# Optimization experiments

Hardware: AMD Instinct MI355X
Metric: run time of the kernel (lower is better)

## Reference

```python
import jax, jax.numpy as jnp
import numpy as np

N, E = 50000, 1600000
D_IN, H, N_REL, D_OUT = 518, 256, 10, 128


def setup_inputs() -> dict:
    key = jax.random.key(0)
    ks = jax.random.split(key, 20)
    def lin(k, fan_in, fan_out):
        bound = 1.0 / np.sqrt(fan_in)
        kw, kb = jax.random.split(k)
        W = jax.random.uniform(kw, (fan_in, fan_out), jnp.float32, -bound, bound)
        b = jax.random.uniform(kb, (fan_out,), jnp.float32, -bound, bound)
        return W, b
    x = jax.random.normal(ks[0], (N, D_IN), jnp.float32)
    edge_index = jax.random.randint(ks[1], (2, E), 0, N, jnp.int32)
    edge_attr = jax.random.randint(ks[2], (E,), 0, N_REL, jnp.int32)
    W_enc1, b_enc1 = lin(ks[3], D_IN, H)
    W_enc2, b_enc2 = lin(ks[4], H, H)
    emb_table = jax.random.normal(ks[5], (N_REL, H // 4), jnp.float32)
    W_g1, b_g1 = lin(ks[6], H, H)
    W_g2, b_g2 = lin(ks[7], H, H)
    W_g3, b_g3 = lin(ks[8], H, H)
    W_h1, b_h1 = lin(ks[9], H, H // 2)
    W_h2, b_h2 = lin(ks[10], H // 2, D_OUT)
    return dict(x=x, edge_index=edge_index, edge_attr=edge_attr,
                W_enc1=W_enc1, b_enc1=b_enc1, W_enc2=W_enc2, b_enc2=b_enc2,
                emb_table=emb_table,
                W_g1=W_g1, b_g1=b_g1, W_g2=W_g2, b_g2=b_g2, W_g3=W_g3, b_g3=b_g3,
                W_h1=W_h1, b_h1=b_h1, W_h2=W_h2, b_h2=b_h2)


def reference(x, edge_index, edge_attr,
              W_enc1, b_enc1, W_enc2, b_enc2, emb_table,
              W_g1, b_g1, W_g2, b_g2, W_g3, b_g3,
              W_h1, b_h1, W_h2, b_h2):
    src, dst = edge_index[0], edge_index[1]
    n = x.shape[0]
    # GCN symmetric normalization with self-loops: deg = 1 + in-degree
    deg = 1.0 + jax.ops.segment_sum(jnp.ones_like(src, jnp.float32), dst, num_segments=n)
    dis = deg ** -0.5                       # [N]
    norm_e = dis[src] * dis[dst]            # [E] edge norm
    self_norm = (dis * dis)[:, None]        # [N,1] self-loop norm

    def gcn(h, W, b):
        hw = h @ W                           # [N,H]
        agg = jax.ops.segment_sum(hw[src] * norm_e[:, None], dst, num_segments=n)
        return agg + hw * self_norm + b

    # node encoder (dropout is identity in eval)
    h = jax.nn.relu(x @ W_enc1 + b_enc1) @ W_enc2 + b_enc2
    _edge_emb = emb_table[edge_attr]         # computed as in original (unused downstream)
    h = jax.nn.relu(gcn(h, W_g1, b_g1))
    h = jax.nn.relu(gcn(h, W_g2, b_g2))
    h = jax.nn.relu(gcn(h, W_g3, b_g3))
    graph_repr = jnp.mean(h, axis=0, keepdims=True)   # batch=None path -> [1,H]
    out = jax.nn.relu(graph_repr @ W_h1 + b_h1) @ W_h2 + b_h2
    return out
```

## Files before the change

### kernel.cpp

```cpp
#include <hip/hip_runtime.h>

#define D_IN 518
#define HD 256
#define KP1 544

typedef __attribute__((ext_vector_type(8))) short bf16x8;
typedef __attribute__((ext_vector_type(4))) float f32x4;
typedef __attribute__((ext_vector_type(4), aligned(4))) float float4u;
typedef __attribute__((ext_vector_type(8))) unsigned short ushort8v;

__device__ __forceinline__ float bf2f(unsigned short u) {
  union { unsigned int i; float f; } v; v.i = ((unsigned int)u) << 16; return v.f;
}
__device__ __forceinline__ unsigned short f2bf(float f) {
  union { float f; unsigned int i; } v; v.f = f;
  unsigned int r = (v.i + 0x7FFFu + ((v.i >> 16) & 1u)) >> 16;
  return (unsigned short)r;
}
__device__ __forceinline__ float rl_f(float x, int j) {
  return __int_as_float(__builtin_amdgcn_readlane(__float_as_int(x), j));
}

__global__ void k_canary(float* __restrict__ out, float code) {
  out[threadIdx.x] = code;
}


__global__ void k_hist(const int* __restrict__ dst, int E, int* __restrict__ cnt) {
  int e = blockIdx.x * blockDim.x + threadIdx.x;
  if (e < E) atomicAdd(&cnt[dst[e]], 1);
}

__global__ void k_blocksum(const int* __restrict__ cnt, int n, int* __restrict__ bsum) {
  __shared__ int red[256];
  const int t = threadIdx.x;
  int v = blockIdx.x * 256 + t;
  red[t] = (v < n) ? cnt[v] : 0;
  __syncthreads();
  for (int d = 128; d > 0; d >>= 1) {
    if (t < d) red[t] += red[t + d];
    __syncthreads();
  }
  if (t == 0) bsum[blockIdx.x] = red[0];
}

__global__ void k_scan_mid(const int* __restrict__ bsum, int nb, int* __restrict__ bex) {
  __shared__ int s[256];
  const int t = threadIdx.x;
  int x = (t < nb) ? bsum[t] : 0;
  s[t] = x;
  __syncthreads();
  for (int d = 1; d < 256; d <<= 1) {
    int v = (t >= d) ? s[t - d] : 0;
    __syncthreads();
    s[t] += v;
    __syncthreads();
  }
  if (t < nb) bex[t] = s[t] - x;
}

__global__ void k_off(const int* __restrict__ cnt, int n, const int* __restrict__ bex,
                      int* __restrict__ off, int* __restrict__ cursor,
                      float* __restrict__ dis) {
  __shared__ int s[256];
  const int t = threadIdx.x;
  const int v = blockIdx.x * 256 + t;
  int c = (v < n) ? cnt[v] : 0;
  s[t] = c;
  __syncthreads();
  for (int d = 1; d < 256; d <<= 1) {
    int x = (t >= d) ? s[t - d] : 0;
    __syncthreads();
    s[t] += x;
    __syncthreads();
  }
  if (v < n) {
    int incl = bex[blockIdx.x] + s[t];
    off[v + 1] = incl;
    cursor[v] = incl - c;
    dis[v] = 1.0f / sqrtf(1.0f + (float)c);
    if (v == 0) off[0] = 0;
  }
}

__global__ void k_fill_range(const int* __restrict__ src, const int* __restrict__ dst, int E,
                             int* __restrict__ cursor, int* __restrict__ csr,
                             int lo, int hi) {
  int e = blockIdx.x * blockDim.x + threadIdx.x;
  if (e < E) {
    int d = dst[e];
    if (d >= lo && d < hi) {
      int p = atomicAdd(&cursor[d], 1);
      csr[p] = src[e];
    }
  }
}


__global__ void k_wt(const float* __restrict__ W, int K, int N, int Kp,
                     unsigned short* __restrict__ Wt) {
  int idx = blockIdx.x * blockDim.x + threadIdx.x;
  if (idx < N * Kp) {
    int n = idx / Kp, k = idx - n * Kp;
    Wt[idx] = (k < K) ? f2bf(W[k * N + n]) : (unsigned short)0;
  }
}

__global__ void k_wt4(const float* __restrict__ a, const float* __restrict__ b,
                      const float* __restrict__ c, const float* __restrict__ d,
                      unsigned short* __restrict__ oa, unsigned short* __restrict__ ob,
                      unsigned short* __restrict__ oc, unsigned short* __restrict__ od) {
  const float* W = (blockIdx.y == 0) ? a : (blockIdx.y == 1) ? b : (blockIdx.y == 2) ? c : d;
  unsigned short* O = (blockIdx.y == 0) ? oa : (blockIdx.y == 1) ? ob : (blockIdx.y == 2) ? oc : od;
  int idx = blockIdx.x * blockDim.x + threadIdx.x;
  int n = idx >> 8, k = idx & 255;
  O[idx] = f2bf(W[k * HD + n]);
}


__global__ __launch_bounds__(256, 2)
void k_gemm_bt(const unsigned short* __restrict__ A, int lda, int M, int K,
               const unsigned short* __restrict__ Bt, int ldb,
               const float* __restrict__ bias, int do_relu,
               unsigned short* __restrict__ C, int ldc) {
  __shared__ unsigned short As[128 * 40];
  __shared__ unsigned short Bs[128 * 40];
  const int tid = threadIdx.x;
  const int lane = tid & 63, wave = tid >> 6;
  const int q = lane >> 4, l15 = lane & 15;
  const int wm = (wave & 1) * 64, wn = (wave >> 1) * 64;
  const int m0 = blockIdx.x * 128, n0 = blockIdx.y * 128;

  f32x4 acc[4][4];
#pragma unroll
  for (int i = 0; i < 4; i++)
#pragma unroll
    for (int j = 0; j < 4; j++) acc[i][j] = f32x4{0.f, 0.f, 0.f, 0.f};

  const int r0 = tid >> 2, kb = tid & 3;
  int gmA0 = m0 + r0;       if (gmA0 >= M) gmA0 = M - 1;
  int gmA1 = m0 + r0 + 64;  if (gmA1 >= M) gmA1 = M - 1;
  const unsigned short* Arow0 = A + (size_t)gmA0 * lda;
  const unsigned short* Arow1 = A + (size_t)gmA1 * lda;
  const unsigned short* Brow0 = Bt + (size_t)(n0 + r0) * ldb;
  const unsigned short* Brow1 = Bt + (size_t)(n0 + r0 + 64) * ldb;
  unsigned short* lA0 = &As[r0 * 40 + kb * 8];
  unsigned short* lA1 = &As[(r0 + 64) * 40 + kb * 8];
  unsigned short* lB0 = &Bs[r0 * 40 + kb * 8];
  unsigned short* lB1 = &Bs[(r0 + 64) * 40 + kb * 8];

  for (int k0 = 0; k0 < K; k0 += 32) {
    __syncthreads();
    const int gk = k0 + kb * 8;
    *(bf16x8*)lA0 = *(const bf16x8*)(Arow0 + gk);
    *(bf16x8*)lA1 = *(const bf16x8*)(Arow1 + gk);
    *(bf16x8*)lB0 = *(const bf16x8*)(Brow0 + gk);
    *(bf16x8*)lB1 = *(const bf16x8*)(Brow1 + gk);
    __syncthreads();

    bf16x8 af[4], bfr[4];
#pragma unroll
    for (int i = 0; i < 4; i++)
      af[i] = *(const bf16x8*)(&As[(wm + i * 16 + l15) * 40 + q * 8]);
#pragma unroll
    for (int j = 0; j < 4; j++)
      bfr[j] = *(const bf16x8*)(&Bs[(wn + j * 16 + l15) * 40 + q * 8]);
#pragma unroll
    for (int i = 0; i < 4; i++)
#pragma unroll
      for (int j = 0; j < 4; j++)
        acc[i][j] = __builtin_amdgcn_mfma_f32_16x16x32_bf16(af[i], bfr[j], acc[i][j], 0, 0, 0);
  }

#pragma unroll
  for (int j = 0; j < 4; j++) {
    const int col = n0 + wn + j * 16 + l15;
    const float bv = bias ? bias[col] : 0.f;
#pragma unroll
    for (int i = 0; i < 4; i++) {
#pragma unroll
      for (int rg = 0; rg < 4; rg++) {
        int gr = m0 + wm + i * 16 + q * 4 + rg;
        if (gr < M) {
          float v = acc[i][j][rg] + bv;
          if (do_relu) v = fmaxf(v, 0.f);
          C[(size_t)gr * ldc + col] = f2bf(v);
        }
      }
    }
  }
}


__global__ __launch_bounds__(256, 2)
void k_gemm_f32in(const float* __restrict__ A, int lda, int M, int Kreal, int Kloop,
                  const unsigned short* __restrict__ Bt, int ldb,
                  const float* __restrict__ bias, int do_relu,
                  unsigned short* __restrict__ C, int ldc) {
  __shared__ unsigned short As[128 * 40];
  __shared__ unsigned short Bs[128 * 40];
  const int tid = threadIdx.x;
  const int lane = tid & 63, wave = tid >> 6;
  const int q = lane >> 4, l15 = lane & 15;
  const int wm = (wave & 1) * 64, wn = (wave >> 1) * 64;
  const int m0 = blockIdx.x * 128, n0 = blockIdx.y * 128;

  f32x4 acc[4][4];
#pragma unroll
  for (int i = 0; i < 4; i++)
#pragma unroll
    for (int j = 0; j < 4; j++) acc[i][j] = f32x4{0.f, 0.f, 0.f, 0.f};

  const int r0 = tid >> 2, kb = tid & 3;
  int gmA0 = m0 + r0;       if (gmA0 >= M) gmA0 = M - 1;
  int gmA1 = m0 + r0 + 64;  if (gmA1 >= M) gmA1 = M - 1;
  const float* Arow0 = A + (size_t)gmA0 * lda;
  const float* Arow1 = A + (size_t)gmA1 * lda;
  const unsigned short* Brow0 = Bt + (size_t)(n0 + r0) * ldb;
  const unsigned short* Brow1 = Bt + (size_t)(n0 + r0 + 64) * ldb;
  unsigned short* lA0 = &As[r0 * 40 + kb * 8];
  unsigned short* lA1 = &As[(r0 + 64) * 40 + kb * 8];
  unsigned short* lB0 = &Bs[r0 * 40 + kb * 8];
  unsigned short* lB1 = &Bs[(r0 + 64) * 40 + kb * 8];

  for (int k0 = 0; k0 < Kloop; k0 += 32) {
    __syncthreads();
    const int gk = k0 + kb * 8;
    if (gk + 8 <= Kreal) {
      float4u a0 = *(const float4u*)(Arow0 + gk);
      float4u a1 = *(const float4u*)(Arow0 + gk + 4);
      float4u b0 = *(const float4u*)(Arow1 + gk);
      float4u b1 = *(const float4u*)(Arow1 + gk + 4);
      bf16x8 t0, t1;
      t0[0] = (short)f2bf(a0.x); t0[1] = (short)f2bf(a0.y);
      t0[2] = (short)f2bf(a0.z); t0[3] = (short)f2bf(a0.w);
      t0[4] = (short)f2bf(a1.x); t0[5] = (short)f2bf(a1.y);
      t0[6] = (short)f2bf(a1.z); t0[7] = (short)f2bf(a1.w);
      t1[0] = (short)f2bf(b0.x); t1[1] = (short)f2bf(b0.y);
      t1[2] = (short)f2bf(b0.z); t1[3] = (short)f2bf(b0.w);
      t1[4] = (short)f2bf(b1.x); t1[5] = (short)f2bf(b1.y);
      t1[6] = (short)f2bf(b1.z); t1[7] = (short)f2bf(b1.w);
      *(bf16x8*)lA0 = t0;
      *(bf16x8*)lA1 = t1;
    } else {
      bf16x8 t0, t1;
#pragma unroll
      for (int t = 0; t < 8; t++) {
        int kk = gk + t;
        t0[t] = (short)((kk < Kreal) ? f2bf(Arow0[kk]) : (unsigned short)0);
        t1[t] = (short)((kk < Kreal) ? f2bf(Arow1[kk]) : (unsigned short)0);
      }
      *(bf16x8*)lA0 = t0;
      *(bf16x8*)lA1 = t1;
    }
    *(bf16x8*)lB0 = *(const bf16x8*)(Brow0 + gk);
    *(bf16x8*)lB1 = *(const bf16x8*)(Brow1 + gk);
    __syncthreads();

    bf16x8 af[4], bfr[4];
#pragma unroll
    for (int i = 0; i < 4; i++)
      af[i] = *(const bf16x8*)(&As[(wm + i * 16 + l15) * 40 + q * 8]);
#pragma unroll
    for (int j = 0; j < 4; j++)
      bfr[j] = *(const bf16x8*)(&Bs[(wn + j * 16 + l15) * 40 + q * 8]);
#pragma unroll
    for (int i = 0; i < 4; i++)
#pragma unroll
      for (int j = 0; j < 4; j++)
        acc[i][j] = __builtin_amdgcn_mfma_f32_16x16x32_bf16(af[i], bfr[j], acc[i][j], 0, 0, 0);
  }

#pragma unroll
  for (int j = 0; j < 4; j++) {
    const int col = n0 + wn + j * 16 + l15;
    const float bv = bias ? bias[col] : 0.f;
#pragma unroll
    for (int i = 0; i < 4; i++) {
#pragma unroll
      for (int rg = 0; rg < 4; rg++) {
        int gr = m0 + wm + i * 16 + q * 4 + rg;
        if (gr < M) {
          float v = acc[i][j][rg] + bv;
          if (do_relu) v = fmaxf(v, 0.f);
          C[(size_t)gr * ldc + col] = f2bf(v);
        }
      }
    }
  }
}


__global__ __launch_bounds__(256)
void k_agg(const unsigned short* __restrict__ hw,
           const int* __restrict__ off, const int* __restrict__ csr,
           const float* __restrict__ dis,
           const float* __restrict__ bias,
           unsigned short* __restrict__ hout, int n) {
  const int wave = threadIdx.x >> 6, lane = threadIdx.x & 63;
  const int v = blockIdx.x * 4 + wave;
  if (v >= n) return;
  const int half = lane >> 5, lc = lane & 31;
  const unsigned short* hwl = hw + lc * 8;
  float a[8];
#pragma unroll
  for (int k = 0; k < 8; ++k) a[k] = 0.f;

  const int e0 = off[v], e1 = off[v + 1];
  for (int e = e0; e < e1; e += 64) {
    int cnt = e1 - e; if (cnt > 64) cnt = 64;
    int sidx = 0; float w = 0.f;
    if (e + lane < e1) { sidx = csr[e + lane]; w = dis[sidx]; }
    int j = 0;
    for (; j + 8 <= cnt; j += 8) {
      int s[4]; float wv[4];
#pragma unroll
      for (int p = 0; p < 4; ++p) {
        int sl = __builtin_amdgcn_readlane(sidx, j + 2 * p);
        int sh = __builtin_amdgcn_readlane(sidx, j + 2 * p + 1);
        float wl = rl_f(w, j + 2 * p);
        float wh = rl_f(w, j + 2 * p + 1);
        s[p]  = half ? sh : sl;
        wv[p] = half ? wh : wl;
      }
      ushort8v h[4];
#pragma unroll
      for (int p = 0; p < 4; ++p)
        h[p] = *(const ushort8v*)(hwl + (size_t)s[p] * HD);
#pragma unroll
      for (int p = 0; p < 4; ++p)
#pragma unroll
        for (int k = 0; k < 8; ++k)
          a[k] += wv[p] * bf2f(h[p][k]);
    }
    for (; j < cnt; j += 2) {
      int sl = __builtin_amdgcn_readlane(sidx, j);
      float wl = rl_f(w, j);
      int sh; float wh;
      if (j + 1 < cnt) { sh = __builtin_amdgcn_readlane(sidx, j + 1); wh = rl_f(w, j + 1); }
      else             { sh = sl; wh = 0.f; }
      int s   = half ? sh : sl;
      float ww = half ? wh : wl;
      ushort8v hv = *(const ushort8v*)(hwl + (size_t)s * HD);
#pragma unroll
      for (int k = 0; k < 8; ++k) a[k] += ww * bf2f(hv[k]);
    }
  }

#pragma unroll
  for (int k = 0; k < 8; ++k) a[k] += __shfl_xor(a[k], 32, 64);

  if (half == 0) {
    const float dv = dis[v], sn = dv * dv;
    ushort8v hs = *(const ushort8v*)(hwl + (size_t)v * HD);
    const int c = lc * 8;
    ushort8v o;
#pragma unroll
    for (int k = 0; k < 8; ++k)
      o[k] = f2bf(fmaxf(dv * a[k] + sn * bf2f(hs[k]) + bias[c + k], 0.f));
    *(ushort8v*)(hout + (size_t)v * HD + c) = o;
  }
}


__global__ void k_colsum(const unsigned short* __restrict__ h, int n, float* __restrict__ gsum) {
  const int t = threadIdx.x;
  const int per = (n + gridDim.x - 1) / gridDim.x;
  const int rs = blockIdx.x * per;
  int re = rs + per; if (re > n) re = n;
  float s = 0.f;
  for (int r = rs; r < re; ++r) s += bf2f(h[(size_t)r * HD + t]);
  atomicAdd(&gsum[t], s);
}

__global__ void k_head(const float* __restrict__ gsum, float invN,
                       const float* __restrict__ Wh1, const float* __restrict__ bh1,
                       const float* __restrict__ Wh2, const float* __restrict__ bh2,
                       float* __restrict__ out) {
  __shared__ float g[256];
  __shared__ float t1[128];
  const int t = threadIdx.x;
  g[t] = gsum[t] * invN;
  g[t + 128] = gsum[t + 128] * invN;
  __syncthreads();
  float s = bh1[t];
  for (int k = 0; k < 256; ++k) s += g[k] * Wh1[k * 128 + t];
  t1[t] = fmaxf(s, 0.f);
  __syncthreads();
  float o = bh2[t];
  for (int j = 0; j < 128; ++j) o += t1[j] * Wh2[j * 128 + t];
  out[t] = o;
}


extern "C" void kernel_launch(void* const* d_in, const int* in_sizes, int n_in,
                              void* d_out, int out_size, void* d_ws, size_t ws_size,
                              hipStream_t stream) {
  float* outp = (float*)d_out;

  const float* x   = (const float*)d_in[0];
  const int* ei    = (const int*)d_in[1];
  const float* W1  = (const float*)d_in[3];
  const float* b1  = (const float*)d_in[4];
  const float* W2  = (const float*)d_in[5];
  const float* b2  = (const float*)d_in[6];
  const float* Wg1 = (const float*)d_in[8];
  const float* bg1 = (const float*)d_in[9];
  const float* Wg2 = (const float*)d_in[10];
  const float* bg2 = (const float*)d_in[11];
  const float* Wg3 = (const float*)d_in[12];
  const float* bg3 = (const float*)d_in[13];
  const float* Wh1 = (const float*)d_in[14];
  const float* bh1 = (const float*)d_in[15];
  const float* Wh2 = (const float*)d_in[16];
  const float* bh2 = (const float*)d_in[17];

  const int n = 50000;
  const int E = 1600000;
  const int nb = (n + 255) / 256;
  const int* srcp = ei;
  const int* dstp = ei + E;

  char* p = (char*)d_ws;
  size_t used = 0;
  auto alloc = [&](size_t bytes) -> char* {
    char* r = p; size_t rb = (bytes + 255) & ~((size_t)255);
    p += rb; used += rb; return r;
  };
  int*   cnt    = (int*)alloc((size_t)n * 4);
  int*   off    = (int*)alloc((size_t)(n + 1) * 4);
  int*   cursor = (int*)alloc((size_t)n * 4);
  float* dis    = (float*)alloc((size_t)n * 4);
  int*   bsum   = (int*)alloc((size_t)nb * 4);
  int*   bex    = (int*)alloc((size_t)nb * 4);
  float* gsum   = (float*)alloc(256 * 4);
  int*   csr    = (int*)alloc((size_t)E * 4);
  unsigned short* W1t  = (unsigned short*)alloc((size_t)HD * KP1 * 2);
  unsigned short* W2t  = (unsigned short*)alloc((size_t)HD * HD * 2);
  unsigned short* Wg1t = (unsigned short*)alloc((size_t)HD * HD * 2);
  unsigned short* Wg2t = (unsigned short*)alloc((size_t)HD * HD * 2);
  unsigned short* Wg3t = (unsigned short*)alloc((size_t)HD * HD * 2);
  unsigned short* P    = (unsigned short*)alloc((size_t)n * HD * 2);
  unsigned short* Q    = (unsigned short*)alloc((size_t)n * HD * 2);

  if (used > ws_size) { k_canary<<<1, 128, 0, stream>>>(outp, 90000.0f); return; }

  hipMemsetAsync(cnt, 0, (size_t)n * 4, stream);
  hipMemsetAsync(gsum, 0, 256 * 4, stream);

  k_hist<<<(E + 255) / 256, 256, 0, stream>>>(dstp, E, cnt);
  k_blocksum<<<nb, 256, 0, stream>>>(cnt, n, bsum);
  k_scan_mid<<<1, 256, 0, stream>>>(bsum, nb, bex);
  k_off<<<nb, 256, 0, stream>>>(cnt, n, bex, off, cursor, dis);
  {
    const int NPASS = 4, span = (n + NPASS - 1) / NPASS;
    for (int i = 0; i < NPASS; ++i) {
      int lo = i * span, hi = lo + span; if (hi > n) hi = n;
      k_fill_range<<<(E + 255) / 256, 256, 0, stream>>>(srcp, dstp, E, cursor, csr, lo, hi);
    }
  }

  k_wt<<<(HD * KP1 + 255) / 256, 256, 0, stream>>>(W1, D_IN, HD, KP1, W1t);
  {
    dim3 g4(HD * HD / 256, 4);
    k_wt4<<<g4, 256, 0, stream>>>(W2, Wg1, Wg2, Wg3, W2t, Wg1t, Wg2t, Wg3t);
  }

  dim3 gg((n + 127) / 128, HD / 128);
  const int ab = (n + 3) / 4;

  k_gemm_f32in<<<gg, 256, 0, stream>>>(x, D_IN, n, D_IN, KP1, W1t, KP1, b1, 1, P, HD);
  k_gemm_bt<<<gg, 256, 0, stream>>>(P, HD, n, HD, W2t, HD, b2, 0, Q, HD);
  k_gemm_bt<<<gg, 256, 0, stream>>>(Q, HD, n, HD, Wg1t, HD, nullptr, 0, P, HD);
  k_agg<<<ab, 256, 0, stream>>>(P, off, csr, dis, bg1, Q, n);
  k_gemm_bt<<<gg, 256, 0, stream>>>(Q, HD, n, HD, Wg2t, HD, nullptr, 0, P, HD);
  k_agg<<<ab, 256, 0, stream>>>(P, off, csr, dis, bg2, Q, n);
  k_gemm_bt<<<gg, 256, 0, stream>>>(Q, HD, n, HD, Wg3t, HD, nullptr, 0, P, HD);
  k_agg<<<ab, 256, 0, stream>>>(P, off, csr, dis, bg3, Q, n);

  k_colsum<<<256, 256, 0, stream>>>(Q, n, gsum);
  k_head<<<1, 128, 0, stream>>>(gsum, 1.0f / (float)n, Wh1, bh1, Wh2, bh2, outp);
}
```

Before: 893.1 us.

## Fold source-degree scaling into GEMM epilogue and simplify aggregation with 16-bit CSR

```diff
diff --git a/kernel.cpp b/kernel.cpp
--- a/kernel.cpp
+++ b/kernel.cpp
@@ -7,7 +7,8 @@
 typedef __attribute__((ext_vector_type(8))) short bf16x8;
 typedef __attribute__((ext_vector_type(4))) float f32x4;
 typedef __attribute__((ext_vector_type(4), aligned(4))) float float4u;
-typedef __attribute__((ext_vector_type(8))) unsigned short ushort8v;
+typedef __attribute__((ext_vector_type(2))) unsigned int uint2v;
+typedef __attribute__((ext_vector_type(4))) unsigned short ushort4v;
 
 __device__ __forceinline__ float bf2f(unsigned short u) {
   union { unsigned int i; float f; } v; v.i = ((unsigned int)u) << 16; return v.f;
@@ -17,9 +18,6 @@
   unsigned int r = (v.i + 0x7FFFu + ((v.i >> 16) & 1u)) >> 16;
   return (unsigned short)r;
 }
-__device__ __forceinline__ float rl_f(float x, int j) {
-  return __int_as_float(__builtin_amdgcn_readlane(__float_as_int(x), j));
-}
 
 __global__ void k_canary(float* __restrict__ out, float code) {
   out[threadIdx.x] = code;
@@ -27,8 +25,14 @@
 
 
 __global__ void k_hist(const int* __restrict__ dst, int E, int* __restrict__ cnt) {
-  int e = blockIdx.x * blockDim.x + threadIdx.x;
-  if (e < E) atomicAdd(&cnt[dst[e]], 1);
+  int e = (blockIdx.x * blockDim.x + threadIdx.x) * 4;
+  if (e < E) {
+    int4 d = *(const int4*)(dst + e);
+    atomicAdd(&cnt[d.x], 1);
+    atomicAdd(&cnt[d.y], 1);
+    atomicAdd(&cnt[d.z], 1);
+    atomicAdd(&cnt[d.w], 1);
+  }
 }
 
 __global__ void k_blocksum(const int* __restrict__ cnt, int n, int* __restrict__ bsum) {
@@ -84,15 +88,16 @@
 }
 
 __global__ void k_fill_range(const int* __restrict__ src, const int* __restrict__ dst, int E,
-                             int* __restrict__ cursor, int* __restrict__ csr,
+                             int* __restrict__ cursor, unsigned short* __restrict__ csr,
                              int lo, int hi) {
-  int e = blockIdx.x * blockDim.x + threadIdx.x;
+  int e = (blockIdx.x * blockDim.x + threadIdx.x) * 4;
   if (e < E) {
-    int d = dst[e];
-    if (d >= lo && d < hi) {
-      int p = atomicAdd(&cursor[d], 1);
-      csr[p] = src[e];
-    }
+    int4 d = *(const int4*)(dst + e);
+    int4 s = *(const int4*)(src + e);
+    if (d.x >= lo && d.x < hi) csr[atomicAdd(&cursor[d.x], 1)] = (unsigned short)s.x;
+    if (d.y >= lo && d.y < hi) csr[atomicAdd(&cursor[d.y], 1)] = (unsigned short)s.y;
+    if (d.z >= lo && d.z < hi) csr[atomicAdd(&cursor[d.z], 1)] = (unsigned short)s.z;
+    if (d.w >= lo && d.w < hi) csr[atomicAdd(&cursor[d.w], 1)] = (unsigned short)s.w;
   }
 }
 
@@ -121,7 +126,8 @@
 __global__ __launch_bounds__(256, 2)
 void k_gemm_bt(const unsigned short* __restrict__ A, int lda, int M, int K,
                const unsigned short* __restrict__ Bt, int ldb,
-               const float* __restrict__ bias, int do_relu,
+               const float* __restrict__ bias, const float* __restrict__ rowscale,
+               int do_relu,
                unsigned short* __restrict__ C, int ldc) {
   __shared__ unsigned short As[128 * 40];
   __shared__ unsigned short Bs[128 * 40];
@@ -182,7 +188,9 @@
       for (int rg = 0; rg < 4; rg++) {
         int gr = m0 + wm + i * 16 + q * 4 + rg;
         if (gr < M) {
-          float v = acc[i][j][rg] + bv;
+          float v = acc[i][j][rg];
+          if (rowscale) v *= rowscale[gr];
+          v += bv;
           if (do_relu) v = fmaxf(v, 0.f);
           C[(size_t)gr * ldc + col] = f2bf(v);
         }
@@ -293,73 +301,76 @@
 
 __global__ __launch_bounds__(256)
 void k_agg(const unsigned short* __restrict__ hw,
-           const int* __restrict__ off, const int* __restrict__ csr,
+           const int* __restrict__ off, const unsigned short* __restrict__ csr,
            const float* __restrict__ dis,
            const float* __restrict__ bias,
            unsigned short* __restrict__ hout, int n) {
   const int wave = threadIdx.x >> 6, lane = threadIdx.x & 63;
   const int v = blockIdx.x * 4 + wave;
   if (v >= n) return;
-  const int half = lane >> 5, lc = lane & 31;
-  const unsigned short* hwl = hw + lc * 8;
-  float a[8];
-#pragma unroll
-  for (int k = 0; k < 8; ++k) a[k] = 0.f;
+  const int cb = lane << 2;
+  float a0 = 0.f, a1 = 0.f, a2 = 0.f, a3 = 0.f;
 
   const int e0 = off[v], e1 = off[v + 1];
   for (int e = e0; e < e1; e += 64) {
     int cnt = e1 - e; if (cnt > 64) cnt = 64;
-    int sidx = 0; float w = 0.f;
-    if (e + lane < e1) { sidx = csr[e + lane]; w = dis[sidx]; }
+    int sidx = 0;
+    if (lane < cnt) sidx = (int)csr[e + lane];
     int j = 0;
     for (; j + 8 <= cnt; j += 8) {
-      int s[4]; float wv[4];
-#pragma unroll
-      for (int p = 0; p < 4; ++p) {
-        int sl = __builtin_amdgcn_readlane(sidx, j + 2 * p);
-        int sh = __builtin_amdgcn_readlane(sidx, j + 2 * p + 1);
-        float wl = rl_f(w, j + 2 * p);
-        float wh = rl_f(w, j + 2 * p + 1);
-        s[p]  = half ? sh : sl;
-        wv[p] = half ? wh : wl;
-      }
-      ushort8v h[4];
-#pragma unroll
-      for (int p = 0; p < 4; ++p)
-        h[p] = *(const ushort8v*)(hwl + (size_t)s[p] * HD);
-#pragma unroll
-      for (int p = 0; p < 4; ++p)
-#pragma unroll
-        for (int k = 0; k < 8; ++k)
-          a[k] += wv[p] * bf2f(h[p][k]);
-    }
-    for (; j < cnt; j += 2) {
-      int sl = __builtin_amdgcn_readlane(sidx, j);
-      float wl = rl_f(w, j);
-      int sh; float wh;
-      if (j + 1 < cnt) { sh = __builtin_amdgcn_readlane(sidx, j + 1); wh = rl_f(w, j + 1); }
-      else             { sh = sl; wh = 0.f; }
-      int s   = half ? sh : sl;
-      float ww = half ? wh : wl;
-      ushort8v hv = *(const ushort8v*)(hwl + (size_t)s * HD);
-#pragma unroll
-      for (int k = 0; k < 8; ++k) a[k] += ww * bf2f(hv[k]);
-    }
-  }
-
-#pragma unroll
-  for (int k = 0; k < 8; ++k) a[k] += __shfl_xor(a[k], 32, 64);
-
-  if (half == 0) {
-    const float dv = dis[v], sn = dv * dv;
-    ushort8v hs = *(const ushort8v*)(hwl + (size_t)v * HD);
-    const int c = lc * 8;
-    ushort8v o;
-#pragma unroll
-    for (int k = 0; k < 8; ++k)
-      o[k] = f2bf(fmaxf(dv * a[k] + sn * bf2f(hs[k]) + bias[c + k], 0.f));
-    *(ushort8v*)(hout + (size_t)v * HD + c) = o;
-  }
+      uint2v d[8];
+#pragma unroll
+      for (int p = 0; p < 8; ++p) {
+        int sp = __builtin_amdgcn_readlane(sidx, j + p);
+        const unsigned short* rowb = hw + ((size_t)sp << 8);
+        d[p] = *(const uint2v*)(rowb + cb);
+      }
+#pragma unroll
+      for (int p = 0; p < 8; ++p) {
+        a0 += __uint_as_float(d[p][0] << 16);
+        a1 += __uint_as_float(d[p][0] & 0xFFFF0000u);
+        a2 += __uint_as_float(d[p][1] << 16);
+        a3 += __uint_as_float(d[p][1] & 0xFFFF0000u);
+      }
+    }
+    if (j < cnt) {
+      uint2v d[8];
+#pragma unroll
+      for (int p = 0; p < 8; ++p) {
+        if (j + p < cnt) {
+          int sp = __builtin_amdgcn_readlane(sidx, j + p);
+          const unsigned short* rowb = hw + ((size_t)sp << 8);
+          d[p] = *(const uint2v*)(rowb + cb);
+        }
+      }
+#pragma unroll
+      for (int p = 0; p < 8; ++p) {
+        if (j + p < cnt) {
+          a0 += __uint_as_float(d[p][0] << 16);
+          a1 += __uint_as_float(d[p][0] & 0xFFFF0000u);
+          a2 += __uint_as_float(d[p][1] << 16);
+          a3 += __uint_as_float(d[p][1] & 0xFFFF0000u);
+        }
+      }
+    }
+  }
+
+  {
+    const unsigned short* rowb = hw + ((size_t)v << 8);
+    uint2v ds_ = *(const uint2v*)(rowb + cb);
+    a0 += __uint_as_float(ds_[0] << 16);
+    a1 += __uint_as_float(ds_[0] & 0xFFFF0000u);
+    a2 += __uint_as_float(ds_[1] << 16);
+    a3 += __uint_as_float(ds_[1] & 0xFFFF0000u);
+  }
+  const float dv = dis[v];
+  const float4u bv = *(const float4u*)(bias + cb);
+  ushort4v o;
+  o[0] = f2bf(fmaxf(dv * a0 + bv.x, 0.f));
+  o[1] = f2bf(fmaxf(dv * a1 + bv.y, 0.f));
+  o[2] = f2bf(fmaxf(dv * a2 + bv.z, 0.f));
+  o[3] = f2bf(fmaxf(dv * a3 + bv.w, 0.f));
+  *(ushort4v*)(hout + ((size_t)v << 8) + cb) = o;
 }
 
 
@@ -434,7 +445,7 @@
   int*   bsum   = (int*)alloc((size_t)nb * 4);
   int*   bex    = (int*)alloc((size_t)nb * 4);
   float* gsum   = (float*)alloc(256 * 4);
-  int*   csr    = (int*)alloc((size_t)E * 4);
+  unsigned short* csr = (unsigned short*)alloc((size_t)E * 2);
   unsigned short* W1t  = (unsigned short*)alloc((size_t)HD * KP1 * 2);
   unsigned short* W2t  = (unsigned short*)alloc((size_t)HD * HD * 2);
   unsigned short* Wg1t = (unsigned short*)alloc((size_t)HD * HD * 2);
@@ -448,15 +459,15 @@
   hipMemsetAsync(cnt, 0, (size_t)n * 4, stream);
   hipMemsetAsync(gsum, 0, 256 * 4, stream);
 
-  k_hist<<<(E + 255) / 256, 256, 0, stream>>>(dstp, E, cnt);
+  k_hist<<<(E / 4 + 255) / 256, 256, 0, stream>>>(dstp, E, cnt);
   k_blocksum<<<nb, 256, 0, stream>>>(cnt, n, bsum);
   k_scan_mid<<<1, 256, 0, stream>>>(bsum, nb, bex);
   k_off<<<nb, 256, 0, stream>>>(cnt, n, bex, off, cursor, dis);
   {
-    const int NPASS = 4, span = (n + NPASS - 1) / NPASS;
+    const int NPASS = 2, span = (n + NPASS - 1) / NPASS;
     for (int i = 0; i < NPASS; ++i) {
       int lo = i * span, hi = lo + span; if (hi > n) hi = n;
-      k_fill_range<<<(E + 255) / 256, 256, 0, stream>>>(srcp, dstp, E, cursor, csr, lo, hi);
+      k_fill_range<<<(E / 4 + 255) / 256, 256, 0, stream>>>(srcp, dstp, E, cursor, csr, lo, hi);
     }
   }
 
@@ -470,12 +481,12 @@
   const int ab = (n + 3) / 4;
 
   k_gemm_f32in<<<gg, 256, 0, stream>>>(x, D_IN, n, D_IN, KP1, W1t, KP1, b1, 1, P, HD);
-  k_gemm_bt<<<gg, 256, 0, stream>>>(P, HD, n, HD, W2t, HD, b2, 0, Q, HD);
-  k_gemm_bt<<<gg, 256, 0, stream>>>(Q, HD, n, HD, Wg1t, HD, nullptr, 0, P, HD);
+  k_gemm_bt<<<gg, 256, 0, stream>>>(P, HD, n, HD, W2t, HD, b2, nullptr, 0, Q, HD);
+  k_gemm_bt<<<gg, 256, 0, stream>>>(Q, HD, n, HD, Wg1t, HD, nullptr, dis, 0, P, HD);
   k_agg<<<ab, 256, 0, stream>>>(P, off, csr, dis, bg1, Q, n);
-  k_gemm_bt<<<gg, 256, 0, stream>>>(Q, HD, n, HD, Wg2t, HD, nullptr, 0, P, HD);
+  k_gemm_bt<<<gg, 256, 0, stream>>>(Q, HD, n, HD, Wg2t, HD, nullptr, dis, 0, P, HD);
   k_agg<<<ab, 256, 0, stream>>>(P, off, csr, dis, bg2, Q, n);
-  k_gemm_bt<<<gg, 256, 0, stream>>>(Q, HD, n, HD, Wg3t, HD, nullptr, 0, P, HD);
+  k_gemm_bt<<<gg, 256, 0, stream>>>(Q, HD, n, HD, Wg3t, HD, nullptr, dis, 0, P, HD);
   k_agg<<<ab, 256, 0, stream>>>(P, off, csr, dis, bg3, Q, n);
 
   k_colsum<<<256, 256, 0, stream>>>(Q, n, gsum);
```

Result: no change. 892.8 us (-0.0%).
